# Performance work log

Measured on AMD Instinct MI355X. Metric: run time of the kernel, lower is better.

## Reference

```python
import math
import jax, jax.numpy as jnp
import numpy as np

L_MAX = 2
B, N, V, P, C, NK = 4, 4096, 4096, 16, 16, 4


def _cg(j1, m1, j2, m2, J, M):
    # Clebsch-Gordan coefficient <j1 m1; j2 m2 | J M> (Racah formula, integer j)
    if M != m1 + m2:
        return 0.0
    f = math.factorial
    pref = (2 * J + 1) * f(j1 + j2 - J) * f(j1 - j2 + J) * f(-j1 + j2 + J) / f(j1 + j2 + J + 1)
    pref *= f(J + M) * f(J - M) * f(j1 - m1) * f(j1 + m1) * f(j2 - m2) * f(j2 + m2)
    t_lo = max(0, j2 - J - m1, j1 + m2 - J)
    t_hi = min(j1 + j2 - J, j1 - m1, j2 + m2)
    s = 0.0
    for t in range(t_lo, t_hi + 1):
        s += (-1) ** t / (f(t) * f(j1 + j2 - J - t) * f(j1 - m1 - t) * f(j2 + m2 - t)
                          * f(J - j2 + m1 + t) * f(J - j1 - m2 + t))
    return math.sqrt(pref) * s


def _Q(J, l, k):
    # Q[M+J, m+l, n+k] = <l m; k n | J M>, shape [2J+1, 2l+1, 2k+1]
    Q = np.zeros((2 * J + 1, 2 * l + 1, 2 * k + 1), np.float32)
    for M in range(-J, J + 1):
        for m in range(-l, l + 1):
            n = M - m
            if -k <= n <= k:
                Q[M + J, m + l, n + k] = _cg(l, m, k, n, J, M)
    return jnp.asarray(Q)


def setup_inputs() -> dict:
    key = jax.random.key(0)
    ks = jax.random.split(key, 8)
    inp = {}
    for l in range(L_MAX + 1):
        inp[f"signal_{l}"] = jax.random.normal(ks[l], (B, N, 2 * l + 1, C), jnp.float32)
        inp[f"kernel_{l}"] = jax.random.normal(ks[3 + l], (B, V, P, 2 * l + 1, NK), jnp.float32)
    pn = jax.random.randint(ks[6], (B, V, P), 0, N)
    pb = jnp.broadcast_to(jnp.arange(B)[:, None, None], (B, V, P))
    inp["patches_idx"] = jnp.stack([pb, pn], axis=-1).astype(jnp.int64)  # [B,V,P,2]
    return inp


def _forward(signals, kernels, patches_idx):
    pb = patches_idx[..., 0]
    pn = patches_idx[..., 1]
    y = {k: [] for k in kernels}
    y_cg = []  # (l, k, ylk)
    for l in sorted(signals):
        sl = signals[l][pb, pn]  # gather_nd -> [B,V,P,2l+1,C]
        for k in sorted(kernels):
            ylk = jnp.einsum('bvpkn,bvpmc->bvmknc', kernels[k], sl)
            b, v, m, kd, n, c = ylk.shape
            ylk = ylk.reshape(b, v, m, kd, n * c)  # [B,V,2l+1,2k+1,NK*C]
            if l > 0:
                y_cg.append((l, k, ylk))
            else:
                y[k].append(ylk[:, :, 0, :, :])  # degree-k output [B,V,2k+1,NK*C]
    # Clebsch-Gordan decomposition of each l>0 pair into degrees J <= L_MAX
    for (l, k, ylk) in y_cg:
        for J in range(abs(l - k), min(l + k, L_MAX) + 1):
            Q = _Q(J, l, k)
            yJ = jnp.einsum('Jmn,bvmnc->bvJc', Q, ylk)
            y.setdefault(J, []).append(yJ)
    return tuple(jnp.concatenate(y[J], axis=-1) for J in sorted(y))


def reference(signal_0, signal_1, signal_2, kernel_0, kernel_1, kernel_2, patches_idx):
    signals = {0: signal_0, 1: signal_1, 2: signal_2}
    kernels = {0: kernel_0, 1: kernel_1, 2: kernel_2}
    return _forward(signals, kernels, patches_idx)
```

## Files before the change

kernel.cpp:

```cpp
#include <hip/hip_runtime.h>

#define N_DIM 4096

constexpr double cfac(int x){ double r=1.0; for(int i=2;i<=x;++i) r*=(double)i; return r; }
constexpr double csqrt_(double x){ double g = x>1.0? x:1.0; for(int i=0;i<200;++i) g=0.5*(g+x/g); return g; }
constexpr double cg_coef(int l,int m,int k,int n,int J,int M){
  if(M != m+n) return 0.0;
  if(n < -k || n > k) return 0.0;
  double pref = (double)(2*J+1)*cfac(l+k-J)*cfac(l-k+J)*cfac(-l+k+J)/cfac(l+k+J+1);
  pref *= cfac(J+M)*cfac(J-M)*cfac(l-m)*cfac(l+m)*cfac(k-n)*cfac(k+n);
  int tlo = 0;
  if(k-J-m > tlo) tlo = k-J-m;
  if(l+n-J > tlo) tlo = l+n-J;
  int thi = l+k-J;
  if(l-m < thi) thi = l-m;
  if(k+n < thi) thi = k+n;
  double s = 0.0;
  for(int t=tlo; t<=thi; ++t){
    double d = cfac(t)*cfac(l+k-J-t)*cfac(l-m-t)*cfac(k+n-t)*cfac(J-k+m+t)*cfac(J-l-n+t);
    s += ((t&1)? -1.0 : 1.0)/d;
  }
  return csqrt_(pref)*s;
}

template<int L_,int K_,int J_> struct QtabT { float a[2*J_+1][2*L_+1]; };
template<int L_,int K_,int J_>
constexpr QtabT<L_,K_,J_> make_q(){
  QtabT<L_,K_,J_> q{};
  for(int M=-J_;M<=J_;++M)
    for(int m=-L_;m<=L_;++m)
      q.a[M+J_][m+L_] = (float)cg_coef(L_,m,K_,M-m,J_,M);
  return q;
}

template<int L_,int K_,int J_,int W_,int CHOFF_>
__device__ __forceinline__ void cg_store(const float (&y)[2*L_+1][2*K_+1],
                                         float* __restrict__ o, size_t bvs, int lane){
  constexpr QtabT<L_,K_,J_> Q = make_q<L_,K_,J_>();
  #pragma unroll
  for(int Mi=0; Mi<2*J_+1; ++Mi){
    float acc = 0.f;
    #pragma unroll
    for(int mi=0; mi<2*L_+1; ++mi){
      const int ni = (Mi-J_) - (mi-L_) + K_;
      if(ni < 0 || ni > 2*K_) continue;
      acc += Q.a[Mi][mi] * y[mi][ni];
    }
    o[(bvs*(2*J_+1) + (size_t)Mi)*W_ + CHOFF_ + lane] = acc;
  }
}

__global__ __launch_bounds__(256, 4)
void conv_kernel(const float* __restrict__ sig0, const float* __restrict__ ker0,
                 const float* __restrict__ sig1, const float* __restrict__ ker1,
                 const float* __restrict__ sig2, const float* __restrict__ ker2,
                 const unsigned* __restrict__ pw, float* __restrict__ out){
  __shared__ __align__(16) float sig_lds[16*144];
  __shared__ __align__(16) float kern_t[16*48];

  const int t    = threadIdx.x;
  const int w    = t >> 6;
  const int lane = t & 63;
  const int bv   = blockIdx.x;
  const size_t bvs = (size_t)bv;
  const int n = lane >> 4, c = lane & 15;

  int row = 0;
  {
    const unsigned probe = (lane < 16) ? pw[2*lane + 1] : 0u;
    const unsigned long long nz = __ballot(probe != 0u);
    const size_t s = (nz == 0ull) ? 2 : 1;
    if(lane < 16){
      const size_t e = ((size_t)bv*16 + lane)*2;
      const int pb = (int)pw[(e+0)*s] & 3;
      const int pn = (int)pw[(e+1)*s] & (N_DIM-1);
      row = pb*N_DIM + pn;
    }
  }

  if(w == 3){
    if(lane < 16){
      float4 v = ((const float4*)(ker0 + bvs*64))[lane];
      float* d = &kern_t[lane*48];
      d[0]=v.x; d[12]=v.y; d[24]=v.z; d[36]=v.w;
    }
    if(lane < 48){
      float4 v = ((const float4*)(ker1 + bvs*192))[lane];
      const int p = lane/3, kd = lane%3;
      float* d = &kern_t[p*48 + 1 + kd];
      d[0]=v.x; d[12]=v.y; d[24]=v.z; d[36]=v.w;
    }
    for(int j=lane; j<80; j+=64){
      float4 v = ((const float4*)(ker2 + bvs*320))[j];
      const int p = j/5, kd = j%5;
      float* d = &kern_t[p*48 + 4 + kd];
      d[0]=v.x; d[12]=v.y; d[24]=v.z; d[36]=v.w;
    }
  } else {
    const int p = lane >> 2, q = lane & 3;
    const size_t ro = (size_t)__shfl(row, p);
    float4* dst = ((float4*)sig_lds) + p*36;
    if(w == 0){
      dst[q]    = ((const float4*)(sig0 + ro*16))[q];
      dst[q+4]  = ((const float4*)(sig1 + ro*48))[q];
      dst[q+8]  = ((const float4*)(sig1 + ro*48))[q+4];
    } else if(w == 1){
      dst[q+12] = ((const float4*)(sig1 + ro*48))[q+8];
      dst[q+16] = ((const float4*)(sig2 + ro*80))[q];
      dst[q+20] = ((const float4*)(sig2 + ro*80))[q+4];
    } else {
      dst[q+24] = ((const float4*)(sig2 + ro*80))[q+8];
      dst[q+28] = ((const float4*)(sig2 + ro*80))[q+12];
      dst[q+32] = ((const float4*)(sig2 + ro*80))[q+16];
    }
  }
  __syncthreads();

  float* o0 = out;
  float* o1 = out + 3145728;
  float* o2 = out + 22020096;

  if(w == 0){
    float y[5][5] = {};
    #pragma unroll
    for(int p=0;p<16;++p){
      float s[5], kk[5];
      #pragma unroll
      for(int i=0;i<5;++i) s[i] = sig_lds[p*144 + (4+i)*16 + c];
      float4 a = *(const float4*)&kern_t[p*48 + n*12 + 4];
      kk[0]=a.x; kk[1]=a.y; kk[2]=a.z; kk[3]=a.w; kk[4]=kern_t[p*48 + n*12 + 8];
      #pragma unroll
      for(int i=0;i<5;++i)
        #pragma unroll
        for(int j=0;j<5;++j) y[i][j] += s[i]*kk[j];
    }
    cg_store<2,2,0,192,128>(y, o0, bvs, lane);
    cg_store<2,2,1,384,320>(y, o1, bvs, lane);
    cg_store<2,2,2,384,320>(y, o2, bvs, lane);
  } else if(w == 1){
    float y0[1][5] = {}, y1[3][5] = {};
    #pragma unroll
    for(int p=0;p<16;++p){
      float s0v = sig_lds[p*144 + c];
      float s[3], kk[5];
      #pragma unroll
      for(int i=0;i<3;++i) s[i] = sig_lds[p*144 + (1+i)*16 + c];
      float4 a = *(const float4*)&kern_t[p*48 + n*12 + 4];
      kk[0]=a.x; kk[1]=a.y; kk[2]=a.z; kk[3]=a.w; kk[4]=kern_t[p*48 + n*12 + 8];
      #pragma unroll
      for(int j=0;j<5;++j){
        y0[0][j] += s0v*kk[j];
        #pragma unroll
        for(int i=0;i<3;++i) y1[i][j] += s[i]*kk[j];
      }
    }
    #pragma unroll
    for(int kd=0;kd<5;++kd) o2[(bvs*5 + kd)*384 + lane] = y0[0][kd];
    cg_store<1,2,1,384,192>(y1, o1, bvs, lane);
    cg_store<1,2,2,384,128>(y1, o2, bvs, lane);
  } else if(w == 2){
    float y11[3][3] = {}, y21[5][3] = {};
    #pragma unroll
    for(int p=0;p<16;++p){
      float s1[3], s2[5], kk[3];
      #pragma unroll
      for(int i=0;i<3;++i) s1[i] = sig_lds[p*144 + (1+i)*16 + c];
      #pragma unroll
      for(int i=0;i<5;++i) s2[i] = sig_lds[p*144 + (4+i)*16 + c];
      #pragma unroll
      for(int j=0;j<3;++j) kk[j] = kern_t[p*48 + n*12 + 1 + j];
      #pragma unroll
      for(int j=0;j<3;++j){
        #pragma unroll
        for(int i=0;i<3;++i) y11[i][j] += s1[i]*kk[j];
        #pragma unroll
        for(int i=0;i<5;++i) y21[i][j] += s2[i]*kk[j];
      }
    }
    cg_store<1,1,0,192, 64>(y11, o0, bvs, lane);
    cg_store<1,1,1,384,128>(y11, o1, bvs, lane);
    cg_store<1,1,2,384, 64>(y11, o2, bvs, lane);
    cg_store<2,1,1,384,256>(y21, o1, bvs, lane);
    cg_store<2,1,2,384,256>(y21, o2, bvs, lane);
  } else {
    float y00 = 0.f, y01[3] = {};
    float y10[3][1] = {}, y20[5][1] = {};
    #pragma unroll
    for(int p=0;p<16;++p){
      float s0v = sig_lds[p*144 + c];
      float sm[8];
      #pragma unroll
      for(int i=0;i<8;++i) sm[i] = sig_lds[p*144 + (1+i)*16 + c];
      float k0v = kern_t[p*48 + n*12];
      float k13[3];
      #pragma unroll
      for(int j=0;j<3;++j) k13[j] = kern_t[p*48 + n*12 + 1 + j];
      y00 += s0v*k0v;
      #pragma unroll
      for(int j=0;j<3;++j) y01[j] += s0v*k13[j];
      #pragma unroll
      for(int i=0;i<3;++i) y10[i][0] += sm[i]*k0v;
      #pragma unroll
      for(int i=0;i<5;++i) y20[i][0] += sm[3+i]*k0v;
    }
    o0[bvs*192 + lane] = y00;
    #pragma unroll
    for(int kd=0;kd<3;++kd) o1[(bvs*3 + kd)*384 + lane] = y01[kd];
    cg_store<1,0,1,384, 64>(y10, o1, bvs, lane);
    cg_store<2,0,2,384,192>(y20, o2, bvs, lane);
  }
}

extern "C" void kernel_launch(void* const* d_in, const int* in_sizes, int n_in,
                              void* d_out, int out_size, void* d_ws, size_t ws_size,
                              hipStream_t stream) {
  const float *s0=nullptr,*s1=nullptr,*s2=nullptr,*k0=nullptr,*k1=nullptr,*k2=nullptr;
  const void* pidx=nullptr;
  if(n_in >= 7){
    s0=(const float*)d_in[0]; k0=(const float*)d_in[1];
    s1=(const float*)d_in[2]; k1=(const float*)d_in[3];
    s2=(const float*)d_in[4]; k2=(const float*)d_in[5];
    pidx=d_in[6];
  }
  for(int i=0;i<n_in;++i){
    switch(in_sizes[i]){
      case 262144:  s0=(const float*)d_in[i]; break;
      case 786432:  s1=(const float*)d_in[i]; break;
      case 1310720: s2=(const float*)d_in[i]; break;
      case 1048576: k0=(const float*)d_in[i]; break;
      case 3145728: k1=(const float*)d_in[i]; break;
      case 5242880: k2=(const float*)d_in[i]; break;
      case 524288:  pidx=d_in[i]; break;
      default: break;
    }
  }

  conv_kernel<<<16384, 256, 0, stream>>>(s0, k0, s1, k1, s2, k2,
                                         (const unsigned*)pidx, (float*)d_out);
}
```

Baseline: 288.7 us.

## Use packed FP32 FMA via inline asm with transposed signal LDS layout

The signal tile in LDS is transposed so each channel's nine m-components sit contiguously with a padded stride. This lets every wave read vectorized v4f/v2f chunks instead of scalar loads. The inner products are rewritten as v_pk_fma_f32 inline-asm operations with op_sel broadcasts, roughly halving the FMA instruction count. Launch bounds also go from 4 to 6 blocks per CU to raise occupancy. The cost is hand-written asm, possible LDS bank conflicts from the new stride, and register pressure under the tighter bound.

```diff
diff --git a/kernel.cpp b/kernel.cpp
--- a/kernel.cpp
+++ b/kernel.cpp
@@ -1,6 +1,14 @@
 #include <hip/hip_runtime.h>
 
 #define N_DIM 4096
+
+typedef float v2f __attribute__((ext_vector_type(2)));
+typedef float v4f __attribute__((ext_vector_type(4)));
+
+#define PK_AB(acc, s, k)   asm("v_pk_fma_f32 %0, %1, %2, %0 op_sel:[0,0,0] op_sel_hi:[0,1,1]" : "+v"(acc) : "v"(s), "v"(k))
+#define PK_AB_H(acc, s, k) asm("v_pk_fma_f32 %0, %1, %2, %0 op_sel:[1,0,0] op_sel_hi:[1,1,1]" : "+v"(acc) : "v"(s), "v"(k))
+#define PK_SB(acc, s, k)   asm("v_pk_fma_f32 %0, %1, %2, %0 op_sel:[0,0,0] op_sel_hi:[1,0,1]" : "+v"(acc) : "v"(s), "v"(k))
+#define PK_SB_H(acc, s, k) asm("v_pk_fma_f32 %0, %1, %2, %0 op_sel:[0,1,0] op_sel_hi:[1,1,1]" : "+v"(acc) : "v"(s), "v"(k))
 
 constexpr double cfac(int x){ double r=1.0; for(int i=2;i<=x;++i) r*=(double)i; return r; }
 constexpr double csqrt_(double x){ double g = x>1.0? x:1.0; for(int i=0;i<200;++i) g=0.5*(g+x/g); return g; }
@@ -50,12 +58,12 @@
   }
 }
 
-__global__ __launch_bounds__(256, 4)
+__global__ __launch_bounds__(256, 6)
 void conv_kernel(const float* __restrict__ sig0, const float* __restrict__ ker0,
                  const float* __restrict__ sig1, const float* __restrict__ ker1,
                  const float* __restrict__ sig2, const float* __restrict__ ker2,
                  const unsigned* __restrict__ pw, float* __restrict__ out){
-  __shared__ __align__(16) float sig_lds[16*144];
+  __shared__ __align__(16) float sig_lds[16*196];
   __shared__ __align__(16) float kern_t[16*48];
 
   const int t    = threadIdx.x;
@@ -99,20 +107,22 @@
   } else {
     const int p = lane >> 2, q = lane & 3;
     const size_t ro = (size_t)__shfl(row, p);
-    float4* dst = ((float4*)sig_lds) + p*36;
+    float* dst = sig_lds + p*196 + 48*q;
+    const float4* r0 = (const float4*)(sig0 + ro*16);
+    const float4* r1 = (const float4*)(sig1 + ro*48);
+    const float4* r2 = (const float4*)(sig2 + ro*80);
+#define WR4(v, mm) { dst[0*12+(mm)]=v.x; dst[1*12+(mm)]=v.y; dst[2*12+(mm)]=v.z; dst[3*12+(mm)]=v.w; }
     if(w == 0){
-      dst[q]    = ((const float4*)(sig0 + ro*16))[q];
-      dst[q+4]  = ((const float4*)(sig1 + ro*48))[q];
-      dst[q+8]  = ((const float4*)(sig1 + ro*48))[q+4];
+      float4 a=r0[q], b=r1[q],    e=r1[q+4];
+      WR4(a,0); WR4(b,1); WR4(e,2);
     } else if(w == 1){
-      dst[q+12] = ((const float4*)(sig1 + ro*48))[q+8];
-      dst[q+16] = ((const float4*)(sig2 + ro*80))[q];
-      dst[q+20] = ((const float4*)(sig2 + ro*80))[q+4];
+      float4 a=r1[q+8], b=r2[q],  e=r2[q+4];
+      WR4(a,3); WR4(b,4); WR4(e,5);
     } else {
-      dst[q+24] = ((const float4*)(sig2 + ro*80))[q+8];
-      dst[q+28] = ((const float4*)(sig2 + ro*80))[q+12];
-      dst[q+32] = ((const float4*)(sig2 + ro*80))[q+16];
-    }
+      float4 a=r2[q+8], b=r2[q+12], e=r2[q+16];
+      WR4(a,6); WR4(b,7); WR4(e,8);
+    }
+#undef WR4
   }
   __syncthreads();
 
@@ -121,88 +131,114 @@
   float* o2 = out + 22020096;
 
   if(w == 0){
-    float y[5][5] = {};
-    #pragma unroll
-    for(int p=0;p<16;++p){
-      float s[5], kk[5];
-      #pragma unroll
-      for(int i=0;i<5;++i) s[i] = sig_lds[p*144 + (4+i)*16 + c];
-      float4 a = *(const float4*)&kern_t[p*48 + n*12 + 4];
-      kk[0]=a.x; kk[1]=a.y; kk[2]=a.z; kk[3]=a.w; kk[4]=kern_t[p*48 + n*12 + 8];
-      #pragma unroll
-      for(int i=0;i<5;++i)
-        #pragma unroll
-        for(int j=0;j<5;++j) y[i][j] += s[i]*kk[j];
-    }
+    v2f yk45[5], yk67[5], c8a={0,0}, c8b={0,0}; float y88=0.f;
+    #pragma unroll
+    for(int i=0;i<5;++i){ yk45[i]=(v2f){0,0}; yk67[i]=(v2f){0,0}; }
+    #pragma unroll
+    for(int p=0;p<16;++p){
+      const float* sp = sig_lds + p*196 + c*12;
+      const float* kp = kern_t  + p*48  + n*12;
+      v4f sB = *(const v4f*)(sp+4);  v2f sC = *(const v2f*)(sp+8);
+      v4f kB = *(const v4f*)(kp+4);  v2f kC = *(const v2f*)(kp+8);
+      v2f s45=sB.xy, s67=sB.zw, k45=kB.xy, k67=kB.zw;
+      PK_AB  (yk45[0], s45, k45); PK_AB  (yk67[0], s45, k67);
+      PK_AB_H(yk45[1], s45, k45); PK_AB_H(yk67[1], s45, k67);
+      PK_AB  (yk45[2], s67, k45); PK_AB  (yk67[2], s67, k67);
+      PK_AB_H(yk45[3], s67, k45); PK_AB_H(yk67[3], s67, k67);
+      PK_AB  (yk45[4], sC,  k45); PK_AB  (yk67[4], sC,  k67);
+      PK_SB  (c8a, s45, kC);      PK_SB  (c8b, s67, kC);
+      y88 += sC.x * kC.x;
+    }
+    float y[5][5];
+    #pragma unroll
+    for(int i=0;i<5;++i){ y[i][0]=yk45[i].x; y[i][1]=yk45[i].y; y[i][2]=yk67[i].x; y[i][3]=yk67[i].y; }
+    y[0][4]=c8a.x; y[1][4]=c8a.y; y[2][4]=c8b.x; y[3][4]=c8b.y; y[4][4]=y88;
     cg_store<2,2,0,192,128>(y, o0, bvs, lane);
     cg_store<2,2,1,384,320>(y, o1, bvs, lane);
     cg_store<2,2,2,384,320>(y, o2, bvs, lane);
   } else if(w == 1){
-    float y0[1][5] = {}, y1[3][5] = {};
-    #pragma unroll
-    for(int p=0;p<16;++p){
-      float s0v = sig_lds[p*144 + c];
-      float s[3], kk[5];
-      #pragma unroll
-      for(int i=0;i<3;++i) s[i] = sig_lds[p*144 + (1+i)*16 + c];
-      float4 a = *(const float4*)&kern_t[p*48 + n*12 + 4];
-      kk[0]=a.x; kk[1]=a.y; kk[2]=a.z; kk[3]=a.w; kk[4]=kern_t[p*48 + n*12 + 8];
-      #pragma unroll
-      for(int j=0;j<5;++j){
-        y0[0][j] += s0v*kk[j];
-        #pragma unroll
-        for(int i=0;i<3;++i) y1[i][j] += s[i]*kk[j];
-      }
-    }
+    v2f a45={0,0}, a67={0,0}, b45[3], b67[3], c8a={0,0}, c8b={0,0};
+    #pragma unroll
+    for(int i=0;i<3;++i){ b45[i]=(v2f){0,0}; b67[i]=(v2f){0,0}; }
+    #pragma unroll
+    for(int p=0;p<16;++p){
+      const float* sp = sig_lds + p*196 + c*12;
+      const float* kp = kern_t  + p*48  + n*12;
+      v4f sA = *(const v4f*)(sp);
+      v4f kB = *(const v4f*)(kp+4);  v2f kC = *(const v2f*)(kp+8);
+      v2f s01=sA.xy, s23=sA.zw, k45=kB.xy, k67=kB.zw;
+      PK_AB  (a45, s01, k45);     PK_AB  (a67, s01, k67);
+      PK_AB_H(b45[0], s01, k45);  PK_AB_H(b67[0], s01, k67);
+      PK_AB  (b45[1], s23, k45);  PK_AB  (b67[1], s23, k67);
+      PK_AB_H(b45[2], s23, k45);  PK_AB_H(b67[2], s23, k67);
+      PK_SB  (c8a, s01, kC);      PK_SB  (c8b, s23, kC);
+    }
+    float y0[1][5] = {{a45.x, a45.y, a67.x, a67.y, c8a.x}};
+    float y1[3][5];
+    y1[0][0]=b45[0].x; y1[0][1]=b45[0].y; y1[0][2]=b67[0].x; y1[0][3]=b67[0].y; y1[0][4]=c8a.y;
+    y1[1][0]=b45[1].x; y1[1][1]=b45[1].y; y1[1][2]=b67[1].x; y1[1][3]=b67[1].y; y1[1][4]=c8b.x;
+    y1[2][0]=b45[2].x; y1[2][1]=b45[2].y; y1[2][2]=b67[2].x; y1[2][3]=b67[2].y; y1[2][4]=c8b.y;
     #pragma unroll
     for(int kd=0;kd<5;++kd) o2[(bvs*5 + kd)*384 + lane] = y0[0][kd];
     cg_store<1,2,1,384,192>(y1, o1, bvs, lane);
     cg_store<1,2,2,384,128>(y1, o2, bvs, lane);
   } else if(w == 2){
-    float y11[3][3] = {}, y21[5][3] = {};
-    #pragma unroll
-    for(int p=0;p<16;++p){
-      float s1[3], s2[5], kk[3];
-      #pragma unroll
-      for(int i=0;i<3;++i) s1[i] = sig_lds[p*144 + (1+i)*16 + c];
-      #pragma unroll
-      for(int i=0;i<5;++i) s2[i] = sig_lds[p*144 + (4+i)*16 + c];
-      #pragma unroll
-      for(int j=0;j<3;++j) kk[j] = kern_t[p*48 + n*12 + 1 + j];
-      #pragma unroll
-      for(int j=0;j<3;++j){
-        #pragma unroll
-        for(int i=0;i<3;++i) y11[i][j] += s1[i]*kk[j];
-        #pragma unroll
-        for(int i=0;i<5;++i) y21[i][j] += s2[i]*kk[j];
-      }
-    }
+    v2f q1[5], r23[8];
+    #pragma unroll
+    for(int i=0;i<5;++i) q1[i]=(v2f){0,0};
+    #pragma unroll
+    for(int i=0;i<8;++i) r23[i]=(v2f){0,0};
+    #pragma unroll
+    for(int p=0;p<16;++p){
+      const float* sp = sig_lds + p*196 + c*12;
+      const float* kp = kern_t  + p*48  + n*12;
+      v4f sA = *(const v4f*)(sp); v4f sB = *(const v4f*)(sp+4); v2f sC = *(const v2f*)(sp+8);
+      v4f kA = *(const v4f*)(kp);
+      v2f s01=sA.xy, s23=sA.zw, s45=sB.xy, s67=sB.zw, k01=kA.xy, k23=kA.zw;
+      PK_SB_H(q1[0], s01, k01); PK_SB_H(q1[1], s23, k01);
+      PK_SB_H(q1[2], s45, k01); PK_SB_H(q1[3], s67, k01);
+      PK_SB_H(q1[4], sC,  k01);
+      PK_AB_H(r23[0], s01, k23);
+      PK_AB  (r23[1], s23, k23); PK_AB_H(r23[2], s23, k23);
+      PK_AB  (r23[3], s45, k23); PK_AB_H(r23[4], s45, k23);
+      PK_AB  (r23[5], s67, k23); PK_AB_H(r23[6], s67, k23);
+      PK_AB  (r23[7], sC,  k23);
+    }
+    float y11[3][3], y21[5][3];
+    y11[0][0]=q1[0].y; y11[0][1]=r23[0].x; y11[0][2]=r23[0].y;
+    y11[1][0]=q1[1].x; y11[1][1]=r23[1].x; y11[1][2]=r23[1].y;
+    y11[2][0]=q1[1].y; y11[2][1]=r23[2].x; y11[2][2]=r23[2].y;
+    y21[0][0]=q1[2].x; y21[0][1]=r23[3].x; y21[0][2]=r23[3].y;
+    y21[1][0]=q1[2].y; y21[1][1]=r23[4].x; y21[1][2]=r23[4].y;
+    y21[2][0]=q1[3].x; y21[2][1]=r23[5].x; y21[2][2]=r23[5].y;
+    y21[3][0]=q1[3].y; y21[3][1]=r23[6].x; y21[3][2]=r23[6].y;
+    y21[4][0]=q1[4].x; y21[4][1]=r23[7].x; y21[4][2]=r23[7].y;
     cg_store<1,1,0,192, 64>(y11, o0, bvs, lane);
     cg_store<1,1,1,384,128>(y11, o1, bvs, lane);
     cg_store<1,1,2,384, 64>(y11, o2, bvs, lane);
     cg_store<2,1,1,384,256>(y21, o1, bvs, lane);
     cg_store<2,1,2,384,256>(y21, o2, bvs, lane);
   } else {
-    float y00 = 0.f, y01[3] = {};
-    float y10[3][1] = {}, y20[5][1] = {};
-    #pragma unroll
-    for(int p=0;p<16;++p){
-      float s0v = sig_lds[p*144 + c];
-      float sm[8];
-      #pragma unroll
-      for(int i=0;i<8;++i) sm[i] = sig_lds[p*144 + (1+i)*16 + c];
-      float k0v = kern_t[p*48 + n*12];
-      float k13[3];
-      #pragma unroll
-      for(int j=0;j<3;++j) k13[j] = kern_t[p*48 + n*12 + 1 + j];
-      y00 += s0v*k0v;
-      #pragma unroll
-      for(int j=0;j<3;++j) y01[j] += s0v*k13[j];
-      #pragma unroll
-      for(int i=0;i<3;++i) y10[i][0] += sm[i]*k0v;
-      #pragma unroll
-      for(int i=0;i<5;++i) y20[i][0] += sm[3+i]*k0v;
-    }
+    v2f tt[5], u={0,0}; float y01_1=0.f;
+    #pragma unroll
+    for(int i=0;i<5;++i) tt[i]=(v2f){0,0};
+    #pragma unroll
+    for(int p=0;p<16;++p){
+      const float* sp = sig_lds + p*196 + c*12;
+      const float* kp = kern_t  + p*48  + n*12;
+      v4f sA = *(const v4f*)(sp); v4f sB = *(const v4f*)(sp+4); v2f sC = *(const v2f*)(sp+8);
+      v4f kA = *(const v4f*)(kp);
+      v2f s01=sA.xy, s23=sA.zw, s45=sB.xy, s67=sB.zw, k01=kA.xy, k23=kA.zw;
+      PK_SB(tt[0], s01, k01); PK_SB(tt[1], s23, k01); PK_SB(tt[2], s45, k01);
+      PK_SB(tt[3], s67, k01); PK_SB(tt[4], sC,  k01);
+      PK_AB(u, s01, k23);
+      y01_1 += sA.x * k01.y;
+    }
+    float y10[3][1], y20[5][1];
+    const float y00 = tt[0].x;
+    y10[0][0]=tt[0].y; y10[1][0]=tt[1].x; y10[2][0]=tt[1].y;
+    y20[0][0]=tt[2].x; y20[1][0]=tt[2].y; y20[2][0]=tt[3].x; y20[3][0]=tt[3].y; y20[4][0]=tt[4].x;
+    float y01[3] = {y01_1, u.x, u.y};
     o0[bvs*192 + lane] = y00;
     #pragma unroll
     for(int kd=0;kd<3;++kd) o1[(bvs*3 + kd)*384 + lane] = y01[kd];
```

Result: no change. 290.1 us (+0.5%).

## Collapse to single-wave blocks computing all degree pairs with packed FMA

Applied to the files above, without the earlier changes.

The kernel now launches 64-thread blocks where one wave computes the full 9x9 signal-by-kernel product instead of splitting the (l,k) pairs across four waves. Signals are stored transposed in LDS so each lane can read contiguous vectors, and accumulation uses inline v_pk_fma_f32 with op_sel to do two FMAs per instruction. The block barrier is removed since only one wave touches LDS. In exchange each wave does more arithmetic and loads, and each block uses more LDS (about 15.6KB per wave versus about 12KB per four waves). That can limit how many waves fit on a CU in a kernel that is likely bound by memory traffic.

```diff
diff --git a/kernel.cpp b/kernel.cpp
--- a/kernel.cpp
+++ b/kernel.cpp
@@ -1,6 +1,14 @@
 #include <hip/hip_runtime.h>
 
 #define N_DIM 4096
+
+typedef float v2f __attribute__((ext_vector_type(2)));
+typedef float v4f __attribute__((ext_vector_type(4)));
+
+#define PK_AB(acc, s, k)   asm("v_pk_fma_f32 %0, %1, %2, %0 op_sel:[0,0,0] op_sel_hi:[0,1,1]" : "+v"(acc) : "v"(s), "v"(k))
+#define PK_AB_H(acc, s, k) asm("v_pk_fma_f32 %0, %1, %2, %0 op_sel:[1,0,0] op_sel_hi:[1,1,1]" : "+v"(acc) : "v"(s), "v"(k))
+#define PK_SB(acc, s, k)   asm("v_pk_fma_f32 %0, %1, %2, %0 op_sel:[0,0,0] op_sel_hi:[1,0,1]" : "+v"(acc) : "v"(s), "v"(k))
+#define PK_SB_H(acc, s, k) asm("v_pk_fma_f32 %0, %1, %2, %0 op_sel:[0,1,0] op_sel_hi:[1,1,1]" : "+v"(acc) : "v"(s), "v"(k))
 
 constexpr double cfac(int x){ double r=1.0; for(int i=2;i<=x;++i) r*=(double)i; return r; }
 constexpr double csqrt_(double x){ double g = x>1.0? x:1.0; for(int i=0;i<200;++i) g=0.5*(g+x/g); return g; }
@@ -50,17 +58,15 @@
   }
 }
 
-__global__ __launch_bounds__(256, 4)
+__global__ __launch_bounds__(64)
 void conv_kernel(const float* __restrict__ sig0, const float* __restrict__ ker0,
                  const float* __restrict__ sig1, const float* __restrict__ ker1,
                  const float* __restrict__ sig2, const float* __restrict__ ker2,
                  const unsigned* __restrict__ pw, float* __restrict__ out){
-  __shared__ __align__(16) float sig_lds[16*144];
+  __shared__ __align__(16) float sig_lds[16*196];
   __shared__ __align__(16) float kern_t[16*48];
 
-  const int t    = threadIdx.x;
-  const int w    = t >> 6;
-  const int lane = t & 63;
+  const int lane = threadIdx.x;
   const int bv   = blockIdx.x;
   const size_t bvs = (size_t)bv;
   const int n = lane >> 4, c = lane & 15;
@@ -78,7 +84,7 @@
     }
   }
 
-  if(w == 3){
+  {
     if(lane < 16){
       float4 v = ((const float4*)(ker0 + bvs*64))[lane];
       float* d = &kern_t[lane*48];
@@ -90,125 +96,123 @@
       float* d = &kern_t[p*48 + 1 + kd];
       d[0]=v.x; d[12]=v.y; d[24]=v.z; d[36]=v.w;
     }
+    #pragma unroll
     for(int j=lane; j<80; j+=64){
       float4 v = ((const float4*)(ker2 + bvs*320))[j];
       const int p = j/5, kd = j%5;
       float* d = &kern_t[p*48 + 4 + kd];
       d[0]=v.x; d[12]=v.y; d[24]=v.z; d[36]=v.w;
     }
-  } else {
+  }
+
+  {
     const int p = lane >> 2, q = lane & 3;
     const size_t ro = (size_t)__shfl(row, p);
-    float4* dst = ((float4*)sig_lds) + p*36;
-    if(w == 0){
-      dst[q]    = ((const float4*)(sig0 + ro*16))[q];
-      dst[q+4]  = ((const float4*)(sig1 + ro*48))[q];
-      dst[q+8]  = ((const float4*)(sig1 + ro*48))[q+4];
-    } else if(w == 1){
-      dst[q+12] = ((const float4*)(sig1 + ro*48))[q+8];
-      dst[q+16] = ((const float4*)(sig2 + ro*80))[q];
-      dst[q+20] = ((const float4*)(sig2 + ro*80))[q+4];
-    } else {
-      dst[q+24] = ((const float4*)(sig2 + ro*80))[q+8];
-      dst[q+28] = ((const float4*)(sig2 + ro*80))[q+12];
-      dst[q+32] = ((const float4*)(sig2 + ro*80))[q+16];
-    }
-  }
-  __syncthreads();
+    float* dst = sig_lds + p*196 + 4*q*12;
+    const float4* r0 = (const float4*)(sig0 + ro*16);
+    const float4* r1 = (const float4*)(sig1 + ro*48);
+    const float4* r2 = (const float4*)(sig2 + ro*80);
+#define WR4(v, mm) { dst[0*12+(mm)]=v.x; dst[1*12+(mm)]=v.y; dst[2*12+(mm)]=v.z; dst[3*12+(mm)]=v.w; }
+    { float4 a=r0[q];    WR4(a,0); }
+    { float4 a=r1[q];    WR4(a,1); }
+    { float4 a=r1[q+4];  WR4(a,2); }
+    { float4 a=r1[q+8];  WR4(a,3); }
+    { float4 a=r2[q];    WR4(a,4); }
+    { float4 a=r2[q+4];  WR4(a,5); }
+    { float4 a=r2[q+8];  WR4(a,6); }
+    { float4 a=r2[q+12]; WR4(a,7); }
+    { float4 a=r2[q+16]; WR4(a,8); }
+#undef WR4
+  }
+
+  v2f t0[5], q1[5], u23[9], a45[9], a67[9], c8[5];
+  #pragma unroll
+  for(int i=0;i<5;++i){ t0[i]=(v2f){0,0}; q1[i]=(v2f){0,0}; c8[i]=(v2f){0,0}; }
+  #pragma unroll
+  for(int i=0;i<9;++i){ u23[i]=(v2f){0,0}; a45[i]=(v2f){0,0}; a67[i]=(v2f){0,0}; }
+
+  #pragma unroll
+  for(int p=0;p<16;++p){
+    const float* sp = sig_lds + p*196 + c*12;
+    const float* kp = kern_t  + p*48  + n*12;
+    v4f sA = *(const v4f*)(sp);   v4f sB = *(const v4f*)(sp+4);  v2f sC = *(const v2f*)(sp+8);
+    v4f kA = *(const v4f*)(kp);   v4f kB = *(const v4f*)(kp+4);  v2f kC = *(const v2f*)(kp+8);
+    v2f s01=sA.xy, s23=sA.zw, s45=sB.xy, s67=sB.zw;
+    v2f k01=kA.xy, k23=kA.zw, k45=kB.xy, k67=kB.zw;
+    PK_SB  (t0[0], s01, k01); PK_SB  (t0[1], s23, k01); PK_SB  (t0[2], s45, k01);
+    PK_SB  (t0[3], s67, k01); PK_SB  (t0[4], sC,  k01);
+    PK_SB_H(q1[0], s01, k01); PK_SB_H(q1[1], s23, k01); PK_SB_H(q1[2], s45, k01);
+    PK_SB_H(q1[3], s67, k01); PK_SB_H(q1[4], sC,  k01);
+    PK_AB  (u23[0], s01, k23); PK_AB_H(u23[1], s01, k23);
+    PK_AB  (u23[2], s23, k23); PK_AB_H(u23[3], s23, k23);
+    PK_AB  (u23[4], s45, k23); PK_AB_H(u23[5], s45, k23);
+    PK_AB  (u23[6], s67, k23); PK_AB_H(u23[7], s67, k23);
+    PK_AB  (u23[8], sC,  k23);
+    PK_AB  (a45[0], s01, k45); PK_AB_H(a45[1], s01, k45);
+    PK_AB  (a45[2], s23, k45); PK_AB_H(a45[3], s23, k45);
+    PK_AB  (a45[4], s45, k45); PK_AB_H(a45[5], s45, k45);
+    PK_AB  (a45[6], s67, k45); PK_AB_H(a45[7], s67, k45);
+    PK_AB  (a45[8], sC,  k45);
+    PK_AB  (a67[0], s01, k67); PK_AB_H(a67[1], s01, k67);
+    PK_AB  (a67[2], s23, k67); PK_AB_H(a67[3], s23, k67);
+    PK_AB  (a67[4], s45, k67); PK_AB_H(a67[5], s45, k67);
+    PK_AB  (a67[6], s67, k67); PK_AB_H(a67[7], s67, k67);
+    PK_AB  (a67[8], sC,  k67);
+    PK_SB  (c8[0], s01, kC);  PK_SB  (c8[1], s23, kC);  PK_SB  (c8[2], s45, kC);
+    PK_SB  (c8[3], s67, kC);  PK_SB  (c8[4], sC,  kC);
+  }
+
+  float y[9][9];
+  #pragma unroll
+  for(int m=0;m<9;++m){
+    y[m][0] = (m<8) ? ((m&1)? t0[m>>1].y : t0[m>>1].x) : t0[4].x;
+    y[m][1] = (m<8) ? ((m&1)? q1[m>>1].y : q1[m>>1].x) : q1[4].x;
+    y[m][2] = u23[m].x;  y[m][3] = u23[m].y;
+    y[m][4] = a45[m].x;  y[m][5] = a45[m].y;
+    y[m][6] = a67[m].x;  y[m][7] = a67[m].y;
+    y[m][8] = (m<8) ? ((m&1)? c8[m>>1].y : c8[m>>1].x) : c8[4].x;
+  }
 
   float* o0 = out;
   float* o1 = out + 3145728;
   float* o2 = out + 22020096;
 
-  if(w == 0){
-    float y[5][5] = {};
-    #pragma unroll
-    for(int p=0;p<16;++p){
-      float s[5], kk[5];
-      #pragma unroll
-      for(int i=0;i<5;++i) s[i] = sig_lds[p*144 + (4+i)*16 + c];
-      float4 a = *(const float4*)&kern_t[p*48 + n*12 + 4];
-      kk[0]=a.x; kk[1]=a.y; kk[2]=a.z; kk[3]=a.w; kk[4]=kern_t[p*48 + n*12 + 8];
-      #pragma unroll
-      for(int i=0;i<5;++i)
-        #pragma unroll
-        for(int j=0;j<5;++j) y[i][j] += s[i]*kk[j];
-    }
-    cg_store<2,2,0,192,128>(y, o0, bvs, lane);
-    cg_store<2,2,1,384,320>(y, o1, bvs, lane);
-    cg_store<2,2,2,384,320>(y, o2, bvs, lane);
-  } else if(w == 1){
-    float y0[1][5] = {}, y1[3][5] = {};
-    #pragma unroll
-    for(int p=0;p<16;++p){
-      float s0v = sig_lds[p*144 + c];
-      float s[3], kk[5];
-      #pragma unroll
-      for(int i=0;i<3;++i) s[i] = sig_lds[p*144 + (1+i)*16 + c];
-      float4 a = *(const float4*)&kern_t[p*48 + n*12 + 4];
-      kk[0]=a.x; kk[1]=a.y; kk[2]=a.z; kk[3]=a.w; kk[4]=kern_t[p*48 + n*12 + 8];
-      #pragma unroll
-      for(int j=0;j<5;++j){
-        y0[0][j] += s0v*kk[j];
-        #pragma unroll
-        for(int i=0;i<3;++i) y1[i][j] += s[i]*kk[j];
-      }
-    }
-    #pragma unroll
-    for(int kd=0;kd<5;++kd) o2[(bvs*5 + kd)*384 + lane] = y0[0][kd];
-    cg_store<1,2,1,384,192>(y1, o1, bvs, lane);
-    cg_store<1,2,2,384,128>(y1, o2, bvs, lane);
-  } else if(w == 2){
-    float y11[3][3] = {}, y21[5][3] = {};
-    #pragma unroll
-    for(int p=0;p<16;++p){
-      float s1[3], s2[5], kk[3];
-      #pragma unroll
-      for(int i=0;i<3;++i) s1[i] = sig_lds[p*144 + (1+i)*16 + c];
-      #pragma unroll
-      for(int i=0;i<5;++i) s2[i] = sig_lds[p*144 + (4+i)*16 + c];
-      #pragma unroll
-      for(int j=0;j<3;++j) kk[j] = kern_t[p*48 + n*12 + 1 + j];
-      #pragma unroll
-      for(int j=0;j<3;++j){
-        #pragma unroll
-        for(int i=0;i<3;++i) y11[i][j] += s1[i]*kk[j];
-        #pragma unroll
-        for(int i=0;i<5;++i) y21[i][j] += s2[i]*kk[j];
-      }
-    }
-    cg_store<1,1,0,192, 64>(y11, o0, bvs, lane);
-    cg_store<1,1,1,384,128>(y11, o1, bvs, lane);
-    cg_store<1,1,2,384, 64>(y11, o2, bvs, lane);
-    cg_store<2,1,1,384,256>(y21, o1, bvs, lane);
-    cg_store<2,1,2,384,256>(y21, o2, bvs, lane);
-  } else {
-    float y00 = 0.f, y01[3] = {};
-    float y10[3][1] = {}, y20[5][1] = {};
-    #pragma unroll
-    for(int p=0;p<16;++p){
-      float s0v = sig_lds[p*144 + c];
-      float sm[8];
-      #pragma unroll
-      for(int i=0;i<8;++i) sm[i] = sig_lds[p*144 + (1+i)*16 + c];
-      float k0v = kern_t[p*48 + n*12];
-      float k13[3];
-      #pragma unroll
-      for(int j=0;j<3;++j) k13[j] = kern_t[p*48 + n*12 + 1 + j];
-      y00 += s0v*k0v;
-      #pragma unroll
-      for(int j=0;j<3;++j) y01[j] += s0v*k13[j];
-      #pragma unroll
-      for(int i=0;i<3;++i) y10[i][0] += sm[i]*k0v;
-      #pragma unroll
-      for(int i=0;i<5;++i) y20[i][0] += sm[3+i]*k0v;
-    }
-    o0[bvs*192 + lane] = y00;
-    #pragma unroll
-    for(int kd=0;kd<3;++kd) o1[(bvs*3 + kd)*384 + lane] = y01[kd];
-    cg_store<1,0,1,384, 64>(y10, o1, bvs, lane);
-    cg_store<2,0,2,384,192>(y20, o2, bvs, lane);
-  }
+  o0[bvs*192 + lane] = y[0][0];
+  #pragma unroll
+  for(int kd=0;kd<3;++kd) o1[(bvs*3 + kd)*384 + lane] = y[0][1+kd];
+  #pragma unroll
+  for(int kd=0;kd<5;++kd) o2[(bvs*5 + kd)*384 + lane] = y[0][4+kd];
+
+  float y10[3][1], y20[5][1], y11[3][3], y21[5][3], y12[3][5], y22[5][5];
+  #pragma unroll
+  for(int i=0;i<3;++i){
+    y10[i][0]=y[1+i][0];
+    #pragma unroll
+    for(int j=0;j<3;++j) y11[i][j]=y[1+i][1+j];
+    #pragma unroll
+    for(int j=0;j<5;++j) y12[i][j]=y[1+i][4+j];
+  }
+  #pragma unroll
+  for(int i=0;i<5;++i){
+    y20[i][0]=y[4+i][0];
+    #pragma unroll
+    for(int j=0;j<3;++j) y21[i][j]=y[4+i][1+j];
+    #pragma unroll
+    for(int j=0;j<5;++j) y22[i][j]=y[4+i][4+j];
+  }
+
+  cg_store<1,0,1,384, 64>(y10, o1, bvs, lane);
+  cg_store<2,0,2,384,192>(y20, o2, bvs, lane);
+  cg_store<1,1,0,192, 64>(y11, o0, bvs, lane);
+  cg_store<1,1,1,384,128>(y11, o1, bvs, lane);
+  cg_store<1,1,2,384, 64>(y11, o2, bvs, lane);
+  cg_store<2,1,1,384,256>(y21, o1, bvs, lane);
+  cg_store<2,1,2,384,256>(y21, o2, bvs, lane);
+  cg_store<1,2,1,384,192>(y12, o1, bvs, lane);
+  cg_store<1,2,2,384,128>(y12, o2, bvs, lane);
+  cg_store<2,2,0,192,128>(y22, o0, bvs, lane);
+  cg_store<2,2,1,384,320>(y22, o1, bvs, lane);
+  cg_store<2,2,2,384,320>(y22, o2, bvs, lane);
 }
 
 extern "C" void kernel_launch(void* const* d_in, const int* in_sizes, int n_in,
@@ -235,6 +239,6 @@
     }
   }
 
-  conv_kernel<<<16384, 256, 0, stream>>>(s0, k0, s1, k1, s2, k2,
-                                         (const unsigned*)pidx, (float*)d_out);
-}
+  conv_kernel<<<16384, 64, 0, stream>>>(s0, k0, s1, k1, s2, k2,
+                                        (const unsigned*)pidx, (float*)d_out);
+}
```

New measurement: 293.6 us. No clear change (+1.7%).
